# Performance work log

Hardware: AMD Instinct MI355X
Metric: run time of the kernel (lower is better)

The kernel has to match this reference:

```python
import jax, jax.numpy as jnp
import numpy as np


def setup_inputs() -> dict:
    key = jax.random.key(0)
    k1, k2, k3 = jax.random.split(key, 3)
    B, C, H, Wd = 32, 768, 32, 32
    K, DQ = 64, 16
    features = jax.random.normal(k1, (B, C, H, Wd), dtype=jnp.float32)
    query = jax.random.normal(k2, (B, DQ, H, Wd), dtype=jnp.float32)
    # Ensemble of 1x1 convs (bias=False): weight [K, dim_query, dim]
    W = jax.random.normal(k3, (K, DQ, C), dtype=jnp.float32) * (1.0 / np.sqrt(C))
    return {"features": features, "query": query, "W": W}


def reference(features, query, W):
    # Ensemble 1x1 conv: key_values [K, B, DQ, H, W]
    kv = jnp.einsum('bchw,kqc->kbqhw', features, W)
    K, B = kv.shape[0], kv.shape[1]
    # cdist between query (b, 1, d) and keys (b, k, d), d = DQ*H*W
    q_flat = query.reshape(B, -1)                       # [B, D]
    k_flat = jnp.moveaxis(kv.reshape(K, B, -1), 0, 1)   # [B, K, D]
    diff = q_flat[:, None, :] - k_flat                  # [B, K, D]
    distance = jnp.sqrt(jnp.sum(diff * diff, axis=-1))  # [B, K]
    # logits = -distance; codes = argmax(logits) == argmin(distance)
    codes = jnp.argmin(distance, axis=-1)               # [B]
    # per-batch gather of selected key_values
    sel = kv[codes, jnp.arange(B)]                      # [B, DQ, H, W]
    commit_loss = jnp.mean((sel - query) ** 2)
    return sel, codes, commit_loss
```

## Files before the change

### kernel.cpp

```cpp
#include <hip/hip_runtime.h>
#include <cstdint>
#include <cstddef>

typedef float f4 __attribute__((ext_vector_type(4)));
typedef float f32x4 __attribute__((ext_vector_type(4)));
typedef short short8 __attribute__((ext_vector_type(8)));
typedef unsigned short u16x8 __attribute__((ext_vector_type(8)));
typedef unsigned short u16x4 __attribute__((ext_vector_type(4)));
typedef unsigned short ushort_t;

#define B_   32
#define C_   768
#define HW_  1024
#define DQ_  16
#define K_   64
#define M_   1024
#define NHWT 16

#define CODE_OFF 524288
#define LOSS_OFF 524320

__device__ __forceinline__ unsigned bf16_rne_bits(float x) {
    unsigned u = __builtin_bit_cast(unsigned, x);
    return (u + 0x7FFFu + ((u >> 16) & 1u)) >> 16;
}
__device__ __forceinline__ float bits_to_f32(unsigned hi16) {
    unsigned u = hi16 << 16;
    return __builtin_bit_cast(float, u);
}
__device__ __forceinline__ void split_bf16(float x, unsigned short& hi, unsigned short& lo) {
    unsigned h = bf16_rne_bits(x);
    hi = (unsigned short)h;
    float r = x - bits_to_f32(h);
    lo = (unsigned short)bf16_rne_bits(r);
}

__global__ __launch_bounds__(256)
void k0_splitF(const float* __restrict__ Fp,
               ushort_t* __restrict__ FhiT, ushort_t* __restrict__ FloT)
{
    __shared__ float tile[64][65];
    const int t = threadIdx.x;
    const int ht = blockIdx.x, ct = blockIdx.y, b = blockIdx.z;

#pragma unroll
    for (int rep = 0; rep < 4; ++rep) {
        int idx = rep * 256 + t;
        int c_l = idx >> 4;
        int hwf = (idx & 15) * 4;
        f4 v = *(const f4*)&Fp[((size_t)b * C_ + ct * 64 + c_l) * HW_ + ht * 64 + hwf];
        tile[c_l][hwf + 0] = v.x;
        tile[c_l][hwf + 1] = v.y;
        tile[c_l][hwf + 2] = v.z;
        tile[c_l][hwf + 3] = v.w;
    }
    __syncthreads();

#pragma unroll
    for (int rep = 0; rep < 2; ++rep) {
        int hw_l = (t >> 3) + rep * 32;
        int cg   = (t & 7) * 8;
        unsigned short hi[8], lo[8];
#pragma unroll
        for (int j = 0; j < 8; ++j)
            split_bf16(tile[cg + j][hw_l], hi[j], lo[j]);
        size_t o = ((size_t)b * HW_ + ht * 64 + hw_l) * C_ + ct * 64 + cg;
        *(u16x8*)&FhiT[o] = *(u16x8*)hi;
        *(u16x8*)&FloT[o] = *(u16x8*)lo;
    }
}

__global__ __launch_bounds__(256)
void k0_splitW(const float* __restrict__ Wp,
               ushort_t* __restrict__ Whi, ushort_t* __restrict__ Wlo)
{
    size_t base = ((size_t)blockIdx.x * 256 + threadIdx.x) * 4;
    f4 v = *(const f4*)&Wp[base];
    unsigned short hi[4], lo[4];
    split_bf16(v.x, hi[0], lo[0]);
    split_bf16(v.y, hi[1], lo[1]);
    split_bf16(v.z, hi[2], lo[2]);
    split_bf16(v.w, hi[3], lo[3]);
    *(u16x4*)&Whi[base] = *(u16x4*)hi;
    *(u16x4*)&Wlo[base] = *(u16x4*)lo;
}

__global__ __launch_bounds__(256)
void k1_mfma(const ushort_t* __restrict__ Whi, const ushort_t* __restrict__ Wlo,
             const ushort_t* __restrict__ FhiT, const ushort_t* __restrict__ FloT,
             const float* __restrict__ Qp, float* __restrict__ partial)
{
    __shared__ ushort_t lds[4][128 * 32];

    const int tid  = threadIdx.x;
    const int wid  = tid >> 6;
    const int lane = tid & 63;
    const int mt = blockIdx.x, hwt = blockIdx.y, b = blockIdx.z;
    const int wm = wid >> 1, wn = wid & 1;

    f32x4 acc[4][4] = {};

    const ushort_t* srcp;
    size_t rowbase;
    if (wid == 0)      { srcp = Whi;  rowbase = (size_t)(mt * 128) * C_; }
    else if (wid == 1) { srcp = Wlo;  rowbase = (size_t)(mt * 128) * C_; }
    else if (wid == 2) { srcp = FhiT; rowbase = ((size_t)b * HW_ + hwt * 128) * C_; }
    else               { srcp = FloT; rowbase = ((size_t)b * HW_ + hwt * 128) * C_; }

    const int rl   = lane >> 2;
    const int slot = lane & 3;
    ushort_t* mytile = &lds[wid][0];

    const int s16 = lane >> 4, c15 = lane & 15;
    int offA[4], offB[4];
#pragma unroll
    for (int i = 0; i < 4; ++i) {
        int ra = wm * 64 + i * 16 + c15;
        offA[i] = ra * 32 + ((s16 ^ ((ra >> 1) & 3)) << 3);
        int rb = wn * 64 + i * 16 + c15;
        offB[i] = rb * 32 + ((s16 ^ ((rb >> 1) & 3)) << 3);
    }

    for (int c0 = 0; c0 < C_; c0 += 32) {
#pragma unroll
        for (int ii = 0; ii < 8; ++ii) {
            int r = ii * 16 + rl;
            int g = slot ^ ((r >> 1) & 3);
            const ushort_t* src = srcp + rowbase + (size_t)r * C_ + c0 + g * 8;
            __builtin_amdgcn_global_load_lds(
                (const __attribute__((address_space(1))) void*)src,
                (__attribute__((address_space(3))) void*)(mytile + ii * 512),
                16, 0, 0);
        }
        __syncthreads();

        short8 ah[4], al[4], bh[4], bl[4];
#pragma unroll
        for (int i = 0; i < 4; ++i) {
            ah[i] = *(const short8*)&lds[0][offA[i]];
            al[i] = *(const short8*)&lds[1][offA[i]];
            bh[i] = *(const short8*)&lds[2][offB[i]];
            bl[i] = *(const short8*)&lds[3][offB[i]];
        }
#pragma unroll
        for (int i = 0; i < 4; ++i)
#pragma unroll
            for (int j = 0; j < 4; ++j) {
                acc[i][j] = __builtin_amdgcn_mfma_f32_16x16x32_bf16(ah[i], bh[j], acc[i][j], 0, 0, 0);
                acc[i][j] = __builtin_amdgcn_mfma_f32_16x16x32_bf16(ah[i], bl[j], acc[i][j], 0, 0, 0);
                acc[i][j] = __builtin_amdgcn_mfma_f32_16x16x32_bf16(al[i], bh[j], acc[i][j], 0, 0, 0);
            }
        __syncthreads();
    }

    float qv[4][4];
#pragma unroll
    for (int j = 0; j < 4; ++j) {
        int hw = hwt * 128 + wn * 64 + j * 16 + c15;
#pragma unroll
        for (int rr = 0; rr < 4; ++rr) {
            int q = s16 * 4 + rr;
            qv[j][rr] = Qp[((size_t)(b * DQ_ + q)) * HW_ + hw];
        }
    }
#pragma unroll
    for (int i = 0; i < 4; ++i) {
        float ssum = 0.f;
#pragma unroll
        for (int j = 0; j < 4; ++j)
#pragma unroll
            for (int rr = 0; rr < 4; ++rr) {
                float d = qv[j][rr] - acc[i][j][rr];
                ssum = fmaf(d, d, ssum);
            }
#pragma unroll
        for (int off = 32; off; off >>= 1) ssum += __shfl_xor(ssum, off);
        if (lane == 0) {
            int k = mt * 8 + wm * 4 + i;
            partial[(((size_t)b * K_ + k) << 4) + hwt * 2 + wn] = ssum;
        }
    }
}

#define BM   256
#define BN   64
#define BC   32
#define NMT  4

__global__ __launch_bounds__(256)
void k1_dist_fp32(const float* __restrict__ Fp, const float* __restrict__ Qp,
                  const float* __restrict__ Wp, float* __restrict__ partial)
{
    __shared__ float w_lds[BC][BM];
    __shared__ float f_lds[BC][BN + 8];
    __shared__ float red[32][8];

    const int tid = threadIdx.x;
    const int mt = blockIdx.x, hwt = blockIdx.y, b = blockIdx.z;
    const int ty = tid >> 3, tx = tid & 7;
    const int m0 = ty * 8, hw0 = tx * 8;

    float acc[8][8];
#pragma unroll
    for (int i = 0; i < 8; ++i)
#pragma unroll
        for (int j = 0; j < 8; ++j) acc[i][j] = 0.f;

    for (int c0 = 0; c0 < C_; c0 += BC) {
#pragma unroll
        for (int i = 0; i < 8; ++i) {
            const int m_l = i * 32 + ty;
            const int c_l = tx * 4;
            const int col = m_l ^ (tx * 4);
            f4 w4 = *(const f4*)&Wp[(size_t)(mt * BM + m_l) * C_ + c0 + c_l];
            w_lds[c_l + 0][col] = w4.x;
            w_lds[c_l + 1][col] = w4.y;
            w_lds[c_l + 2][col] = w4.z;
            w_lds[c_l + 3][col] = w4.w;
        }
        {
            const int c = tid >> 3;
            const int hw = (tid & 7) * 8;
            const float* src = &Fp[((size_t)b * C_ + c0 + c) * HW_ + (size_t)hwt * BN + hw];
            *(f4*)&f_lds[c][hw]     = *(const f4*)src;
            *(f4*)&f_lds[c][hw + 4] = *(const f4*)(src + 4);
        }
        __syncthreads();

#pragma unroll 4
        for (int cc = 0; cc < BC; ++cc) {
            const int sw = ((cc >> 2) & 7) * 4;
            const int colA = m0 ^ sw;
            f4 w0 = *(const f4*)&w_lds[cc][colA];
            f4 w1 = *(const f4*)&w_lds[cc][colA ^ 4];
            f4 g0 = *(const f4*)&f_lds[cc][hw0];
            f4 g1 = *(const f4*)&f_lds[cc][hw0 + 4];
            const float wa[8] = {w0.x, w0.y, w0.z, w0.w, w1.x, w1.y, w1.z, w1.w};
            const float fv[8] = {g0.x, g0.y, g0.z, g0.w, g1.x, g1.y, g1.z, g1.w};
#pragma unroll
            for (int i = 0; i < 8; ++i)
#pragma unroll
                for (int j = 0; j < 8; ++j)
                    acc[i][j] = fmaf(wa[i], fv[j], acc[i][j]);
        }
        __syncthreads();
    }

    const int q0 = (ty & 1) * 8;
    float s = 0.f;
#pragma unroll
    for (int i = 0; i < 8; ++i) {
        const float* qp = &Qp[((size_t)b * DQ_ + q0 + i) * HW_ + (size_t)hwt * BN + hw0];
        f4 qa = *(const f4*)qp;
        f4 qb = *(const f4*)(qp + 4);
        float d;
        d = qa.x - acc[i][0]; s = fmaf(d, d, s);
        d = qa.y - acc[i][1]; s = fmaf(d, d, s);
        d = qa.z - acc[i][2]; s = fmaf(d, d, s);
        d = qa.w - acc[i][3]; s = fmaf(d, d, s);
        d = qb.x - acc[i][4]; s = fmaf(d, d, s);
        d = qb.y - acc[i][5]; s = fmaf(d, d, s);
        d = qb.z - acc[i][6]; s = fmaf(d, d, s);
        d = qb.w - acc[i][7]; s = fmaf(d, d, s);
    }
    red[ty][tx] = s;
    __syncthreads();
    if (tid < 16) {
        float t = 0.f;
#pragma unroll
        for (int r = 0; r < 2; ++r)
#pragma unroll
            for (int x = 0; x < 8; ++x) t += red[tid * 2 + r][x];
        partial[((size_t)b * K_ + mt * 16 + tid) * NHWT + hwt] = t;
    }
}

__global__ __launch_bounds__(1024)
void k2_select(const float* __restrict__ partial, float* __restrict__ out,
               int* __restrict__ codes_ws)
{
    const int tid = threadIdx.x;
    const int b = tid >> 5, kk = tid & 31;
    float s0 = 0.f, s1 = 0.f;
#pragma unroll
    for (int h = 0; h < NHWT; ++h) {
        s0 += partial[((size_t)b * K_ + kk) * NHWT + h];
        s1 += partial[((size_t)b * K_ + kk + 32) * NHWT + h];
    }
    float bv = s0; int bk = kk;
    if (s1 < bv) { bv = s1; bk = kk + 32; }
#pragma unroll
    for (int m = 16; m >= 1; m >>= 1) {
        float ov = __shfl_xor(bv, m);
        int   ok = __shfl_xor(bk, m);
        if (ov < bv || (ov == bv && ok < bk)) { bv = ov; bk = ok; }
    }
    __shared__ float mins[32];
    if (kk == 0) {
        out[CODE_OFF + b] = (float)bk;
        codes_ws[b] = bk;
        mins[b] = bv;
    }
    __syncthreads();
    if (tid == 0) {
        float t = 0.f;
#pragma unroll
        for (int i = 0; i < 32; ++i) t += mins[i];
        out[LOSS_OFF] = t * (1.0f / 524288.0f);
    }
}

#define BN3 128
#define BC3 32

__global__ __launch_bounds__(256)
void k3_sel(const float* __restrict__ Fp, const float* __restrict__ Wp,
            const int* __restrict__ codes_ws, float* __restrict__ out)
{
    __shared__ float f_lds[BC3][BN3];
    __shared__ float w_lds[DQ_][33];

    const int tid = threadIdx.x;
    const int b = blockIdx.x >> 3, hwt = blockIdx.x & 7;
    const int code = codes_ws[b];
    const int q = tid >> 4;
    const int hw0 = (tid & 15) * 8;

    float a[8] = {0.f, 0.f, 0.f, 0.f, 0.f, 0.f, 0.f, 0.f};

    for (int c0 = 0; c0 < C_; c0 += BC3) {
        if (tid < 128) {
            const int qq = tid >> 3, c4 = (tid & 7) * 4;
            f4 w4 = *(const f4*)&Wp[((size_t)code * DQ_ + qq) * C_ + c0 + c4];
            w_lds[qq][c4 + 0] = w4.x;
            w_lds[qq][c4 + 1] = w4.y;
            w_lds[qq][c4 + 2] = w4.z;
            w_lds[qq][c4 + 3] = w4.w;
        }
        {
            const int c = tid >> 3;
            const int hw = (tid & 7) * 16;
            const float* src = &Fp[((size_t)b * C_ + c0 + c) * HW_ + (size_t)hwt * BN3 + hw];
            *(f4*)&f_lds[c][hw]      = *(const f4*)(src);
            *(f4*)&f_lds[c][hw + 4]  = *(const f4*)(src + 4);
            *(f4*)&f_lds[c][hw + 8]  = *(const f4*)(src + 8);
            *(f4*)&f_lds[c][hw + 12] = *(const f4*)(src + 12);
        }
        __syncthreads();
#pragma unroll 4
        for (int cc = 0; cc < BC3; ++cc) {
            const float wv = w_lds[q][cc];
            f4 g0 = *(const f4*)&f_lds[cc][hw0];
            f4 g1 = *(const f4*)&f_lds[cc][hw0 + 4];
            a[0] = fmaf(wv, g0.x, a[0]);
            a[1] = fmaf(wv, g0.y, a[1]);
            a[2] = fmaf(wv, g0.z, a[2]);
            a[3] = fmaf(wv, g0.w, a[3]);
            a[4] = fmaf(wv, g1.x, a[4]);
            a[5] = fmaf(wv, g1.y, a[5]);
            a[6] = fmaf(wv, g1.z, a[6]);
            a[7] = fmaf(wv, g1.w, a[7]);
        }
        __syncthreads();
    }

    float* dst = &out[((size_t)b * DQ_ + q) * HW_ + (size_t)hwt * BN3 + hw0];
    f4 o0 = {a[0], a[1], a[2], a[3]};
    f4 o1 = {a[4], a[5], a[6], a[7]};
    *(f4*)dst = o0;
    *(f4*)(dst + 4) = o1;
}

extern "C" void kernel_launch(void* const* d_in, const int* in_sizes, int n_in,
                              void* d_out, int out_size, void* d_ws, size_t ws_size,
                              hipStream_t stream)
{
    const float* Fp = (const float*)d_in[0];
    const float* Qp = (const float*)d_in[1];
    const float* Wp = (const float*)d_in[2];
    float* out = (float*)d_out;

    const size_t FT_ELEMS = (size_t)B_ * HW_ * C_;
    const size_t W_ELEMS  = (size_t)M_ * C_;
    const size_t PART_OFF = 4 * FT_ELEMS + 4 * W_ELEMS;
    const size_t CODE_WS  = PART_OFF + (size_t)B_ * K_ * NHWT * 4;
    const size_t NEED     = CODE_WS + 128;

    if (ws_size >= NEED) {
        ushort_t* FhiT = (ushort_t*)d_ws;
        ushort_t* FloT = FhiT + FT_ELEMS;
        ushort_t* Whi  = FloT + FT_ELEMS;
        ushort_t* Wlo  = Whi + W_ELEMS;
        float* partial = (float*)((char*)d_ws + PART_OFF);
        int* codes_ws  = (int*)((char*)d_ws + CODE_WS);

        k0_splitF<<<dim3(16, 12, B_), 256, 0, stream>>>(Fp, FhiT, FloT);
        k0_splitW<<<dim3(W_ELEMS / 1024), 256, 0, stream>>>(Wp, Whi, Wlo);
        k1_mfma<<<dim3(8, 8, B_), 256, 0, stream>>>(Whi, Wlo, FhiT, FloT, Qp, partial);
        k2_select<<<1, 1024, 0, stream>>>(partial, out, codes_ws);
        k3_sel<<<dim3(B_ * 8), 256, 0, stream>>>(Fp, Wp, codes_ws, out);
    } else {
        float* partial = (float*)d_ws;
        int* codes_ws  = (int*)((char*)d_ws + (size_t)B_ * K_ * NHWT * 4);
        k1_dist_fp32<<<dim3(NMT, NHWT, B_), 256, 0, stream>>>(Fp, Qp, Wp, partial);
        k2_select<<<1, 1024, 0, stream>>>(partial, out, codes_ws);
        k3_sel<<<dim3(B_ * 8), 256, 0, stream>>>(Fp, Wp, codes_ws, out);
    }
}
```

Measured before the change: 378.2 us.

## Rewrite split-bf16 GEMM as 256x256-tile 8-wave double-buffered MFMA kernel

Replaces the 128x128-tile, 4-wave MFMA kernel with a 512-thread kernel that computes 256x256 output tiles and uses K=64 double-buffered LDS stages. Global-to-LDS loads for the next stage are interleaved with MFMA quads, and s_setprio and sched_barrier are used to keep the matrix pipe busy. The three hi/lo product terms are flattened into a single 36-step K loop instead of three MFMAs per step. Block indices are remapped so that neighbouring blocks share data in cache. The larger tile raises reuse per loaded byte, at the cost of more accumulator registers and only 512 blocks in the grid.

Measured after the change: 349.9 us. 7.5% less time.

```diff
diff --git a/kernel.cpp b/kernel.cpp
--- a/kernel.cpp
+++ b/kernel.cpp
@@ -85,99 +85,195 @@
     *(u16x4*)&Wlo[base] = *(u16x4*)lo;
 }
 
-__global__ __launch_bounds__(256)
-void k1_mfma(const ushort_t* __restrict__ Whi, const ushort_t* __restrict__ Wlo,
-             const ushort_t* __restrict__ FhiT, const ushort_t* __restrict__ FloT,
-             const float* __restrict__ Qp, float* __restrict__ partial)
-{
-    __shared__ ushort_t lds[4][128 * 32];
+#define NKT 36
+
+__global__ __launch_bounds__(512, 2)
+void k1_mfma8(const ushort_t* __restrict__ Whi, const ushort_t* __restrict__ Wlo,
+              const ushort_t* __restrict__ FhiT, const ushort_t* __restrict__ FloT,
+              const float* __restrict__ Qp, float* __restrict__ partial)
+{
+    __shared__ ushort_t lds[2][32768];
 
     const int tid  = threadIdx.x;
-    const int wid  = tid >> 6;
+    const int w    = tid >> 6;
     const int lane = tid & 63;
-    const int mt = blockIdx.x, hwt = blockIdx.y, b = blockIdx.z;
-    const int wm = wid >> 1, wn = wid & 1;
-
-    f32x4 acc[4][4] = {};
-
-    const ushort_t* srcp;
-    size_t rowbase;
-    if (wid == 0)      { srcp = Whi;  rowbase = (size_t)(mt * 128) * C_; }
-    else if (wid == 1) { srcp = Wlo;  rowbase = (size_t)(mt * 128) * C_; }
-    else if (wid == 2) { srcp = FhiT; rowbase = ((size_t)b * HW_ + hwt * 128) * C_; }
-    else               { srcp = FloT; rowbase = ((size_t)b * HW_ + hwt * 128) * C_; }
-
-    const int rl   = lane >> 2;
-    const int slot = lane & 3;
-    ushort_t* mytile = &lds[wid][0];
-
-    const int s16 = lane >> 4, c15 = lane & 15;
-    int offA[4], offB[4];
-#pragma unroll
-    for (int i = 0; i < 4; ++i) {
-        int ra = wm * 64 + i * 16 + c15;
-        offA[i] = ra * 32 + ((s16 ^ ((ra >> 1) & 3)) << 3);
-        int rb = wn * 64 + i * 16 + c15;
-        offB[i] = rb * 32 + ((s16 ^ ((rb >> 1) & 3)) << 3);
-    }
-
-    for (int c0 = 0; c0 < C_; c0 += 32) {
+
+    const int bid = blockIdx.x;
+    const int idx = (bid & 7) * 64 + (bid >> 3);
+    const int mt  = idx & 3;
+    const int hwt = (idx >> 2) & 3;
+    const int b   = idx >> 4;
+
+    const int wm = w >> 2, wn = w & 3;
+
+    const bool isA    = (w < 4);
+    const int  wrow0  = (w & 3) * 64;
+    const int  srow   = lane >> 3;
+    const int  sslot  = (lane & 7) ^ srow;
+    const int  regoff = isA ? 0 : 16384;
+    const size_t abase = (size_t)(mt * 256) * C_;
+    const size_t bbase = ((size_t)b * HW_ + hwt * 256) * C_;
+
+    const int c15 = lane & 15, d0 = lane >> 4;
+    int offA[8][2], offB[4][2];
+#pragma unroll
+    for (int i = 0; i < 8; ++i) {
+        int m = wm * 128 + i * 16 + c15;
+#pragma unroll
+        for (int kh = 0; kh < 2; ++kh) {
+            int d = kh * 4 + d0;
+            offA[i][kh] = m * 64 + ((d ^ (m & 7)) << 3);
+        }
+    }
+#pragma unroll
+    for (int j = 0; j < 4; ++j) {
+        int n = wn * 64 + j * 16 + c15;
+#pragma unroll
+        for (int kh = 0; kh < 2; ++kh) {
+            int d = kh * 4 + d0;
+            offB[j][kh] = 16384 + n * 64 + ((d ^ (n & 7)) << 3);
+        }
+    }
+
+    f32x4 acc[8][4] = {};
+
+    {
+        const ushort_t* sb = isA ? (Whi + abase) : (FhiT + bbase);
 #pragma unroll
         for (int ii = 0; ii < 8; ++ii) {
-            int r = ii * 16 + rl;
-            int g = slot ^ ((r >> 1) & 3);
-            const ushort_t* src = srcp + rowbase + (size_t)r * C_ + c0 + g * 8;
+            const ushort_t* g = sb + (size_t)(wrow0 + ii * 8 + srow) * C_ + sslot * 8;
             __builtin_amdgcn_global_load_lds(
-                (const __attribute__((address_space(1))) void*)src,
-                (__attribute__((address_space(3))) void*)(mytile + ii * 512),
+                (const __attribute__((address_space(1))) void*)g,
+                (__attribute__((address_space(3))) void*)&lds[0][regoff + (wrow0 + ii * 8) * 64],
                 16, 0, 0);
         }
-        __syncthreads();
-
-        short8 ah[4], al[4], bh[4], bl[4];
-#pragma unroll
-        for (int i = 0; i < 4; ++i) {
-            ah[i] = *(const short8*)&lds[0][offA[i]];
-            al[i] = *(const short8*)&lds[1][offA[i]];
-            bh[i] = *(const short8*)&lds[2][offB[i]];
-            bl[i] = *(const short8*)&lds[3][offB[i]];
-        }
-#pragma unroll
-        for (int i = 0; i < 4; ++i)
-#pragma unroll
-            for (int j = 0; j < 4; ++j) {
-                acc[i][j] = __builtin_amdgcn_mfma_f32_16x16x32_bf16(ah[i], bh[j], acc[i][j], 0, 0, 0);
-                acc[i][j] = __builtin_amdgcn_mfma_f32_16x16x32_bf16(ah[i], bl[j], acc[i][j], 0, 0, 0);
-                acc[i][j] = __builtin_amdgcn_mfma_f32_16x16x32_bf16(al[i], bh[j], acc[i][j], 0, 0, 0);
+    }
+    asm volatile("s_waitcnt vmcnt(0)" ::: "memory");
+    __builtin_amdgcn_s_barrier();
+
+    short8 af[4][2], bf0[2][2], bf1[2][2];
+
+#define STAGE2(II)                                                                              \
+    if (do_stage) {                                                                             \
+        const ushort_t* g0 = sb + (size_t)(wrow0 + (II) * 8 + srow) * C_ + sslot * 8;           \
+        __builtin_amdgcn_global_load_lds(                                                       \
+            (const __attribute__((address_space(1))) void*)g0,                                  \
+            (__attribute__((address_space(3))) void*)(Lnext + regoff + (wrow0 + (II) * 8) * 64),\
+            16, 0, 0);                                                                          \
+        const ushort_t* g1 = sb + (size_t)(wrow0 + (II) * 8 + 8 + srow) * C_ + sslot * 8;       \
+        __builtin_amdgcn_global_load_lds(                                                       \
+            (const __attribute__((address_space(1))) void*)g1,                                  \
+            (__attribute__((address_space(3))) void*)(Lnext + regoff + (wrow0 + (II) * 8 + 8) * 64),\
+            16, 0, 0);                                                                          \
+    }
+
+#define QUAD(I0, J0, BF)                                                                        \
+    _Pragma("unroll")                                                                           \
+    for (int i4 = 0; i4 < 4; ++i4)                                                              \
+        _Pragma("unroll")                                                                       \
+        for (int j2 = 0; j2 < 2; ++j2)                                                          \
+            _Pragma("unroll")                                                                   \
+            for (int kh = 0; kh < 2; ++kh)                                                      \
+                acc[(I0) + i4][(J0) + j2] = __builtin_amdgcn_mfma_f32_16x16x32_bf16(            \
+                    af[i4][kh], BF[j2][kh], acc[(I0) + i4][(J0) + j2], 0, 0, 0);
+
+#define PRE_MFMA()                                          \
+    __builtin_amdgcn_s_barrier();                           \
+    asm volatile("s_waitcnt lgkmcnt(0)" ::: "memory");      \
+    __builtin_amdgcn_sched_barrier(0);                      \
+    __builtin_amdgcn_s_setprio(1);
+
+#define POST_MFMA()                                         \
+    __builtin_amdgcn_s_setprio(0);                          \
+    __builtin_amdgcn_sched_barrier(0);                      \
+    __builtin_amdgcn_s_barrier();
+
+    for (int t = 0; t < NKT; ++t) {
+        const int cur = t & 1;
+        const ushort_t* L = &lds[cur][0];
+        ushort_t* Lnext = &lds[cur ^ 1][0];
+
+        const bool do_stage = (t + 1 < NKT);
+        const int tt = do_stage ? (t + 1) : 0;
+        const int term = (tt >= 24) ? 2 : ((tt >= 12) ? 1 : 0);
+        const int c0 = (tt - term * 12) * 64;
+        const ushort_t* sb;
+        if (isA) sb = ((term == 1) ? Wlo : Whi) + abase + c0;
+        else     sb = ((term == 2) ? FloT : FhiT) + bbase + c0;
+
+#pragma unroll
+        for (int i4 = 0; i4 < 4; ++i4)
+#pragma unroll
+            for (int kh = 0; kh < 2; ++kh)
+                af[i4][kh] = *(const short8*)&L[offA[i4][kh]];
+#pragma unroll
+        for (int j2 = 0; j2 < 2; ++j2)
+#pragma unroll
+            for (int kh = 0; kh < 2; ++kh)
+                bf0[j2][kh] = *(const short8*)&L[offB[j2][kh]];
+        STAGE2(0)
+        PRE_MFMA()
+        QUAD(0, 0, bf0)
+        POST_MFMA()
+
+#pragma unroll
+        for (int j2 = 0; j2 < 2; ++j2)
+#pragma unroll
+            for (int kh = 0; kh < 2; ++kh)
+                bf1[j2][kh] = *(const short8*)&L[offB[2 + j2][kh]];
+        STAGE2(2)
+        PRE_MFMA()
+        QUAD(0, 2, bf1)
+        POST_MFMA()
+
+#pragma unroll
+        for (int i4 = 0; i4 < 4; ++i4)
+#pragma unroll
+            for (int kh = 0; kh < 2; ++kh)
+                af[i4][kh] = *(const short8*)&L[offA[4 + i4][kh]];
+        STAGE2(4)
+        PRE_MFMA()
+        QUAD(4, 2, bf1)
+        POST_MFMA()
+
+        STAGE2(6)
+        __builtin_amdgcn_s_barrier();
+        __builtin_amdgcn_sched_barrier(0);
+        __builtin_amdgcn_s_setprio(1);
+        QUAD(4, 0, bf0)
+        __builtin_amdgcn_s_setprio(0);
+        __builtin_amdgcn_sched_barrier(0);
+        asm volatile("s_waitcnt vmcnt(0)" ::: "memory");
+        __builtin_amdgcn_s_barrier();
+    }
+#undef STAGE2
+#undef QUAD
+#undef PRE_MFMA
+#undef POST_MFMA
+
+    float qv[4][4];
+#pragma unroll
+    for (int j = 0; j < 4; ++j) {
+        const int hw = hwt * 256 + wn * 64 + j * 16 + c15;
+#pragma unroll
+        for (int r = 0; r < 4; ++r)
+            qv[j][r] = Qp[(size_t)(b * DQ_ + d0 * 4 + r) * HW_ + hw];
+    }
+#pragma unroll
+    for (int i = 0; i < 8; ++i) {
+        float s = 0.f;
+#pragma unroll
+        for (int j = 0; j < 4; ++j)
+#pragma unroll
+            for (int r = 0; r < 4; ++r) {
+                float d = qv[j][r] - acc[i][j][r];
+                s = fmaf(d, d, s);
             }
-        __syncthreads();
-    }
-
-    float qv[4][4];
-#pragma unroll
-    for (int j = 0; j < 4; ++j) {
-        int hw = hwt * 128 + wn * 64 + j * 16 + c15;
-#pragma unroll
-        for (int rr = 0; rr < 4; ++rr) {
-            int q = s16 * 4 + rr;
-            qv[j][rr] = Qp[((size_t)(b * DQ_ + q)) * HW_ + hw];
-        }
-    }
-#pragma unroll
-    for (int i = 0; i < 4; ++i) {
-        float ssum = 0.f;
-#pragma unroll
-        for (int j = 0; j < 4; ++j)
-#pragma unroll
-            for (int rr = 0; rr < 4; ++rr) {
-                float d = qv[j][rr] - acc[i][j][rr];
-                ssum = fmaf(d, d, ssum);
-            }
-#pragma unroll
-        for (int off = 32; off; off >>= 1) ssum += __shfl_xor(ssum, off);
+#pragma unroll
+        for (int off = 32; off; off >>= 1) s += __shfl_xor(s, off);
         if (lane == 0) {
-            int k = mt * 8 + wm * 4 + i;
-            partial[(((size_t)b * K_ + k) << 4) + hwt * 2 + wn] = ssum;
+            const int k = mt * 16 + wm * 8 + i;
+            partial[((size_t)b * K_ + k) * NHWT + hwt * 4 + wn] = s;
         }
     }
 }
@@ -396,7 +492,7 @@
 
         k0_splitF<<<dim3(16, 12, B_), 256, 0, stream>>>(Fp, FhiT, FloT);
         k0_splitW<<<dim3(W_ELEMS / 1024), 256, 0, stream>>>(Wp, Whi, Wlo);
-        k1_mfma<<<dim3(8, 8, B_), 256, 0, stream>>>(Whi, Wlo, FhiT, FloT, Qp, partial);
+        k1_mfma8<<<dim3(512), 512, 0, stream>>>(Whi, Wlo, FhiT, FloT, Qp, partial);
         k2_select<<<1, 1024, 0, stream>>>(partial, out, codes_ws);
         k3_sel<<<dim3(B_ * 8), 256, 0, stream>>>(Fp, Wp, codes_ws, out);
     } else {
```
